# Performance work log

Hardware: AMD Instinct MI355X
Metric: run time of the kernel (lower is better)

Reference implementation:

```python
import jax, jax.numpy as jnp
import numpy as np

EMBED_DIM = 768
NUM_HEADS = 12
HEAD_DIM = EMBED_DIM // NUM_HEADS
SCALING = HEAD_DIM ** -0.5
B, N = 4, 2048


def setup_inputs() -> dict:
    key = jax.random.key(0)
    k_x, k_wqkv, k_bqkv, k_wo, k_bo = jax.random.split(key, 5)
    s = EMBED_DIM ** -0.5
    return {
        "x_q": jax.random.normal(k_x, (B, N, EMBED_DIM), dtype=jnp.float32),
        # torch Linear weight layout: (out_features, in_features)
        "w_qkv": jax.random.normal(k_wqkv, (3 * EMBED_DIM, EMBED_DIM), dtype=jnp.float32) * s,
        "b_qkv": jax.random.normal(k_bqkv, (3 * EMBED_DIM,), dtype=jnp.float32) * s,
        "w_out": jax.random.normal(k_wo, (EMBED_DIM, EMBED_DIM), dtype=jnp.float32) * s,
        "b_out": jax.random.normal(k_bo, (EMBED_DIM,), dtype=jnp.float32) * s,
    }


def reference(x_q, w_qkv, b_qkv, w_out, b_out):
    b_sz, n, _ = x_q.shape
    # qkv projection: x @ W^T + b -> (B, N, 3E)
    qkv = jnp.einsum("bne,fe->bnf", x_q, w_qkv) + b_qkv
    # reshape to (B, N, 3, H, D) then move heads: (B, H, 3, N, D)
    qkv = qkv.reshape(b_sz, n, 3, NUM_HEADS, HEAD_DIM).transpose(0, 3, 2, 1, 4)
    q, k, v = qkv[:, :, 0], qkv[:, :, 1], qkv[:, :, 2]
    q = q * SCALING
    # scores (B, H, N, N); att_m == 'Aug' adds constant +1 bias
    attn = jnp.einsum("bhqd,bhkd->bhqk", q, k) + 1.0
    attn = jax.nn.softmax(attn, axis=-1)
    # attn_dropout p=0.0 -> identity
    out = jnp.einsum("bhqk,bhkd->bhqd", attn, v)
    out = out.transpose(0, 2, 1, 3).reshape(b_sz, n, EMBED_DIM)
    return jnp.einsum("bne,fe->bnf", out, w_out) + b_out
```

## Files before the change

kernel.cpp:

```cpp
#include <hip/hip_runtime.h>

typedef unsigned short u16;
typedef unsigned int   u32;
typedef __bf16 bf16x4 __attribute__((ext_vector_type(4)));
typedef __bf16 bf16x8 __attribute__((ext_vector_type(8)));
typedef float  f32x4  __attribute__((ext_vector_type(4)));

__device__ __forceinline__ u16 f2bf(float f) {
  u32 u = __float_as_uint(f);
  u32 r = (u + 0x7fffu + ((u >> 16) & 1u)) >> 16;
  return (u16)r;
}

__device__ __forceinline__ float fexp2(float x) {
  return __builtin_amdgcn_exp2f(x);
}

typedef const __attribute__((address_space(1))) u32* gp1;
typedef __attribute__((address_space(3))) u32* lp3;
__device__ __forceinline__ void gload16(const void* g, void* l) {
  __builtin_amdgcn_global_load_lds((gp1)g, (lp3)l, 16, 0, 0);
}

__device__ __forceinline__ f32x4 mfma16(bf16x8 a, bf16x8 b, f32x4 c) {
  return __builtin_amdgcn_mfma_f32_16x16x32_bf16(a, b, c, 0, 0, 0);
}

__device__ __forceinline__ int swz8(int r) { return (r ^ (r >> 3)) & 7; }

__global__ __launch_bounds__(256) void cast_all(const float* __restrict__ x,
                                                const float* __restrict__ wqkv,
                                                const float* __restrict__ wo,
                                                uint4* __restrict__ dst) {
  int i = blockIdx.x * 256 + threadIdx.x;
  if (i >= 1081344) return;
  const float* s;
  int j;
  if (i < 786432)       { s = x;    j = i; }
  else if (i < 1007616) { s = wqkv; j = i - 786432; }
  else                  { s = wo;   j = i - 1007616; }
  const float4* s4 = (const float4*)s;
  float4 a = s4[2 * j], b = s4[2 * j + 1];
  uint4 o;
  o.x = (u32)f2bf(a.x) | ((u32)f2bf(a.y) << 16);
  o.y = (u32)f2bf(a.z) | ((u32)f2bf(a.w) << 16);
  o.z = (u32)f2bf(b.x) | ((u32)f2bf(b.y) << 16);
  o.w = (u32)f2bf(b.z) | ((u32)f2bf(b.w) << 16);
  dst[i] = o;
}

__global__ __launch_bounds__(256) void gemm_qkv(
    const u16* __restrict__ A, const u16* __restrict__ Bm,
    const float* __restrict__ bias,
    u16* __restrict__ Q, u16* __restrict__ K, u16* __restrict__ V) {
  __shared__ u16 As[2][128 * 64];
  __shared__ u16 Bs[2][128 * 64];
  const int tid = threadIdx.x, w = tid >> 6, l = tid & 63;
  const int lr = l & 15, lg = l >> 4;
  int id = blockIdx.x;
  int bi = (id & 7) * 144 + (id >> 3);
  const int m0 = (bi / 18) * 128, n0 = (bi % 18) * 128;
  const int wr = (w >> 1) * 64, wc = (w & 1) * 64;
  f32x4 acc[4][4] = {};

#define GSTAGE(buf, kt)                                                        \
  do {                                                                         \
    const u16* Ab = A + m0 * 768 + (kt);                                       \
    const u16* Bb = Bm + n0 * 768 + (kt);                                      \
    _Pragma("unroll") for (int i = 0; i < 4; ++i) {                            \
      int c = i * 256 + tid;                                                   \
      int r = c >> 3, q = c & 7;                                               \
      int qs = (q ^ swz8(r)) << 3;                                             \
      gload16(Ab + r * 768 + qs, (char*)As[buf] + c * 16);                     \
      gload16(Bb + r * 768 + qs, (char*)Bs[buf] + c * 16);                     \
    }                                                                          \
  } while (0)

  GSTAGE(0, 0);
  __syncthreads();

  for (int t = 0; t < 12; ++t) {
    const int buf = t & 1;
    if (t < 11) GSTAGE(buf ^ 1, (t + 1) * 64);
    bf16x8 af[4][2], bfr[4][2];
#pragma unroll
    for (int m = 0; m < 4; ++m) {
      int row = wr + m * 16 + lr;
      int sw = swz8(row);
#pragma unroll
      for (int ks = 0; ks < 2; ++ks)
        af[m][ks] = *(const bf16x8*)((char*)As[buf] + row * 128 +
                                     (((ks * 4 + lg) ^ sw) << 4));
    }
#pragma unroll
    for (int n = 0; n < 4; ++n) {
      int row = wc + n * 16 + lr;
      int sw = swz8(row);
#pragma unroll
      for (int ks = 0; ks < 2; ++ks)
        bfr[n][ks] = *(const bf16x8*)((char*)Bs[buf] + row * 128 +
                                      (((ks * 4 + lg) ^ sw) << 4));
    }
    __builtin_amdgcn_s_setprio(1);
#pragma unroll
    for (int ks = 0; ks < 2; ++ks)
#pragma unroll
      for (int m = 0; m < 4; ++m)
#pragma unroll
        for (int n = 0; n < 4; ++n)
          acc[m][n] = mfma16(af[m][ks], bfr[n][ks], acc[m][n]);
    __builtin_amdgcn_s_setprio(0);
    __syncthreads();
  }

#pragma unroll
  for (int n = 0; n < 4; ++n) {
    int f = n0 + wc + n * 16 + lr;
    float bv = bias[f];
    int three = f / 768;
    int hd = f - three * 768;
    int h = hd >> 6, dd = hd & 63;
    if (three == 2) {
#pragma unroll
      for (int m = 0; m < 4; ++m) {
        int row0 = m0 + wr + m * 16 + lg * 4;
        int b2 = row0 >> 11, ns = row0 & 2047;
        ushort4 pk;
        pk.x = f2bf(acc[m][n][0] + bv);
        pk.y = f2bf(acc[m][n][1] + bv);
        pk.z = f2bf(acc[m][n][2] + bv);
        pk.w = f2bf(acc[m][n][3] + bv);
        *(ushort4*)&V[((size_t)(b2 * 12 + h) * 64 + dd) * 2048 + ns] = pk;
      }
    } else {
      u16* dst = (three == 0) ? Q : K;
      float sc = (three == 0) ? 0.125f * 1.44269504f : 1.0f;
#pragma unroll
      for (int m = 0; m < 4; ++m) {
        int row0 = m0 + wr + m * 16 + lg * 4;
#pragma unroll
        for (int j = 0; j < 4; ++j) {
          int row = row0 + j;
          int b2 = row >> 11, ns = row & 2047;
          float val = (acc[m][n][j] + bv) * sc;
          dst[(((b2 * 12 + h) * 2048 + ns) << 6) + dd] = f2bf(val);
        }
      }
    }
  }
}

__global__ __launch_bounds__(256, 3) void attn_kernel(
    const u16* __restrict__ Q, const u16* __restrict__ K,
    const u16* __restrict__ Vt, u16* __restrict__ O) {
  __shared__ u16 Ks[3][64 * 64];
  __shared__ u16 Vs[3][64 * 64];
  const int tid = threadIdx.x, w = tid >> 6, l = tid & 63;
  const int lr = l & 15, lg = l >> 4;
  int d0i = blockIdx.x;
  int bi = (d0i & 7) * 96 + (d0i >> 3);
  int qt = bi & 15, h = (bi >> 4) % 12, b = bi / 192;
  const u16* Qp = Q + ((size_t)(b * 12 + h) * 2048 + qt * 128) * 64;
  const u16* Kp = K + (size_t)(b * 12 + h) * 2048 * 64;
  const u16* Vp = Vt + (size_t)(b * 12 + h) * 64 * 2048;
  u16* Op = O + (size_t)(b * 2048 + qt * 128) * 768 + h * 64;

  bf16x8 aq[2][2];
#pragma unroll
  for (int mt = 0; mt < 2; ++mt)
#pragma unroll
    for (int ks = 0; ks < 2; ++ks)
      aq[mt][ks] = *(const bf16x8*)&Qp[(w * 32 + mt * 16 + lr) * 64 + ks * 32 + lg * 8];

  bf16x8 vone;
#pragma unroll
  for (int i = 0; i < 8; ++i) vone[i] = (__bf16)1.0f;

  f32x4 aO[2][4] = {};
  f32x4 sacc[2] = {};

#define STAGEP(kb, vb, kt)                                                     \
  do {                                                                         \
    const u16* Kt = Kp + (kt) * 4096;                                          \
    const u16* Vg = Vp + (kt) * 64;                                            \
    _Pragma("unroll") for (int i = 0; i < 2; ++i) {                            \
      int c = i * 256 + tid;                                                   \
      int r = c >> 3, q = c & 7;                                               \
      int qs = (q ^ swz8(r)) << 3;                                             \
      gload16(Kt + r * 64 + qs, (char*)(kb) + c * 16);                         \
      gload16(Vg + r * 2048 + qs, (char*)(vb) + c * 16);                       \
    }                                                                          \
  } while (0)

  u16 *kc = Ks[0], *kn = Ks[1], *kf = Ks[2];
  u16 *vc = Vs[0], *vn = Vs[1], *vf = Vs[2];

  STAGEP(kc, vc, 0);
  STAGEP(kn, vn, 1);

  for (int kt = 0; kt < 32; ++kt) {
    if (kt == 31) asm volatile("s_waitcnt vmcnt(0)" ::: "memory");
    else          asm volatile("s_waitcnt vmcnt(4)" ::: "memory");
    __builtin_amdgcn_s_barrier();
    __builtin_amdgcn_sched_barrier(0);
    if (kt < 30) STAGEP(kf, vf, kt + 2);

    f32x4 S[2][4] = {};
    __builtin_amdgcn_s_setprio(1);
#pragma unroll
    for (int nt = 0; nt < 4; ++nt) {
      int row = nt * 16 + lr;
      int sw = swz8(row);
#pragma unroll
      for (int ks = 0; ks < 2; ++ks) {
        bf16x8 a = *(const bf16x8*)((char*)kc + row * 128 +
                                    (((ks * 4 + lg) ^ sw) << 4));
        S[0][nt] = mfma16(a, aq[0][ks], S[0][nt]);
        S[1][nt] = mfma16(a, aq[1][ks], S[1][nt]);
      }
    }
    __builtin_amdgcn_s_setprio(0);

    bf16x8 ap[2][2];
#pragma unroll
    for (int mt = 0; mt < 2; ++mt) {
      f32x4 pe[4];
#pragma unroll
      for (int nt = 0; nt < 4; ++nt)
#pragma unroll
        for (int j = 0; j < 4; ++j) pe[nt][j] = fexp2(S[mt][nt][j]);
#pragma unroll
      for (int ks = 0; ks < 2; ++ks) {
        bf16x8 f;
#pragma unroll
        for (int j = 0; j < 4; ++j) {
          f[j]     = (__bf16)pe[2 * ks][j];
          f[4 + j] = (__bf16)pe[2 * ks + 1][j];
        }
        ap[mt][ks] = f;
      }
    }

    __builtin_amdgcn_s_setprio(1);
#pragma unroll
    for (int ks = 0; ks < 2; ++ks) {
      sacc[0] = mfma16(ap[0][ks], vone, sacc[0]);
      sacc[1] = mfma16(ap[1][ks], vone, sacc[1]);
#pragma unroll
      for (int dt = 0; dt < 4; ++dt) {
        int row = dt * 16 + lr;
        int sw = swz8(row);
        char* vrow = (char*)vc + row * 128 + (lg & 1) * 8;
        bf16x4 lo = *(const bf16x4*)(vrow + (((ks * 4 + (lg >> 1)) ^ sw) << 4));
        bf16x4 hi = *(const bf16x4*)(vrow + (((ks * 4 + 2 + (lg >> 1)) ^ sw) << 4));
        bf16x8 bv = __builtin_shufflevector(lo, hi, 0, 1, 2, 3, 4, 5, 6, 7);
        aO[0][dt] = mfma16(ap[0][ks], bv, aO[0][dt]);
        aO[1][dt] = mfma16(ap[1][ks], bv, aO[1][dt]);
      }
    }
    __builtin_amdgcn_s_setprio(0);

    u16* tk = kc; kc = kn; kn = kf; kf = tk;
    u16* tv = vc; vc = vn; vn = vf; vf = tv;
  }

#pragma unroll
  for (int mt = 0; mt < 2; ++mt) {
    f32x4 rinv;
#pragma unroll
    for (int j = 0; j < 4; ++j) rinv[j] = 1.0f / sacc[mt][j];
#pragma unroll
    for (int dt = 0; dt < 4; ++dt)
#pragma unroll
      for (int j = 0; j < 4; ++j) {
        int row = w * 32 + mt * 16 + lg * 4 + j;
        Op[(size_t)row * 768 + dt * 16 + lr] = f2bf(aO[mt][dt][j] * rinv[j]);
      }
  }
}

__global__ __launch_bounds__(256) void gemm_out(
    const u16* __restrict__ A, const u16* __restrict__ Bm,
    const float* __restrict__ bias, float* __restrict__ C) {
  __shared__ u16 As[2][128 * 64];
  __shared__ u16 Bs[2][128 * 64];
  const int tid = threadIdx.x, w = tid >> 6, l = tid & 63;
  const int lr = l & 15, lg = l >> 4;
  int id = blockIdx.x;
  int bi = (id & 7) * 48 + (id >> 3);
  const int m0 = (bi / 6) * 128, n0 = (bi % 6) * 128;
  const int wr = (w >> 1) * 64, wc = (w & 1) * 64;
  f32x4 acc[4][4] = {};

  GSTAGE(0, 0);
  __syncthreads();

  for (int t = 0; t < 12; ++t) {
    const int buf = t & 1;
    if (t < 11) GSTAGE(buf ^ 1, (t + 1) * 64);
    bf16x8 af[4][2], bfr[4][2];
#pragma unroll
    for (int m = 0; m < 4; ++m) {
      int row = wr + m * 16 + lr;
      int sw = swz8(row);
#pragma unroll
      for (int ks = 0; ks < 2; ++ks)
        af[m][ks] = *(const bf16x8*)((char*)As[buf] + row * 128 +
                                     (((ks * 4 + lg) ^ sw) << 4));
    }
#pragma unroll
    for (int n = 0; n < 4; ++n) {
      int row = wc + n * 16 + lr;
      int sw = swz8(row);
#pragma unroll
      for (int ks = 0; ks < 2; ++ks)
        bfr[n][ks] = *(const bf16x8*)((char*)Bs[buf] + row * 128 +
                                      (((ks * 4 + lg) ^ sw) << 4));
    }
    __builtin_amdgcn_s_setprio(1);
#pragma unroll
    for (int ks = 0; ks < 2; ++ks)
#pragma unroll
      for (int m = 0; m < 4; ++m)
#pragma unroll
        for (int n = 0; n < 4; ++n)
          acc[m][n] = mfma16(af[m][ks], bfr[n][ks], acc[m][n]);
    __builtin_amdgcn_s_setprio(0);
    __syncthreads();
  }

#pragma unroll
  for (int n = 0; n < 4; ++n) {
    int f = n0 + wc + n * 16 + lr;
    float bv = bias[f];
#pragma unroll
    for (int m = 0; m < 4; ++m) {
      int row0 = m0 + wr + m * 16 + lg * 4;
#pragma unroll
      for (int j = 0; j < 4; ++j) {
        int row = row0 + j;
        C[(size_t)row * 768 + f] = acc[m][n][j] + bv;
      }
    }
  }
}

extern "C" void kernel_launch(void* const* d_in, const int* in_sizes, int n_in,
                              void* d_out, int out_size, void* d_ws, size_t ws_size,
                              hipStream_t stream) {
  const float* x     = (const float*)d_in[0];
  const float* w_qkv = (const float*)d_in[1];
  const float* b_qkv = (const float*)d_in[2];
  const float* w_out = (const float*)d_in[3];
  const float* b_out = (const float*)d_in[4];

  char* ws = (char*)d_ws;
  u16* xb    = (u16*)(ws + 0);
  u16* wqkvb = (u16*)(ws + 12582912);
  u16* wob   = (u16*)(ws + 16121856);
  u16* qb    = (u16*)(ws + 17301504);
  u16* kb    = (u16*)(ws + 29884416);
  u16* vb    = (u16*)(ws + 42467328);
  u16* ob    = (u16*)(ws + 55050240);

  cast_all<<<4224, 256, 0, stream>>>(x, w_qkv, w_out, (uint4*)ws);

  gemm_qkv<<<1152, 256, 0, stream>>>(xb, wqkvb, b_qkv, qb, kb, vb);
  attn_kernel<<<768, 256, 0, stream>>>(qb, kb, vb, ob);
  gemm_out<<<384, 256, 0, stream>>>(ob, wob, b_out, (float*)d_out);
}
```

Measured before the change: 132.2 us.

## Triple-buffer GEMM K-loops with BK=32 and halve gemm_out N tile

Both projection GEMMs move from a double-buffered BK=64 loop with __syncthreads to a three-stage ring of BK=32 tiles. Each iteration waits with an explicit vmcnt and a single barrier, then prefetches two stages ahead, so global loads overlap more MFMA work and LDS per block shrinks, letting three blocks fit per CU. gemm_out also changes from 128x128 to 128x64 output tiles and launches 768 blocks, improving CU fill for the small output GEMM. The cost is twice as many barriers per K, a new row-pair swizzled LDS layout that must be conflict-free, and hand-tuned vmcnt counts that must match the number of outstanding loads.

New measurement: 138.7 us. 4.9% more time.

```diff
diff --git a/kernel.cpp b/kernel.cpp
--- a/kernel.cpp
+++ b/kernel.cpp
@@ -49,12 +49,13 @@
   dst[i] = o;
 }
 
-__global__ __launch_bounds__(256) void gemm_qkv(
+
+__global__ __launch_bounds__(256, 3) void gemm_qkv(
     const u16* __restrict__ A, const u16* __restrict__ Bm,
     const float* __restrict__ bias,
     u16* __restrict__ Q, u16* __restrict__ K, u16* __restrict__ V) {
-  __shared__ u16 As[2][128 * 64];
-  __shared__ u16 Bs[2][128 * 64];
+  __shared__ u16 As[3][64 * 64];
+  __shared__ u16 Bs[3][64 * 64];
   const int tid = threadIdx.x, w = tid >> 6, l = tid & 63;
   const int lr = l & 15, lg = l >> 4;
   int id = blockIdx.x;
@@ -63,54 +64,56 @@
   const int wr = (w >> 1) * 64, wc = (w & 1) * 64;
   f32x4 acc[4][4] = {};
 
-#define GSTAGE(buf, kt)                                                        \
+#define QSTAGE(ab, bb, kt)                                                     \
   do {                                                                         \
     const u16* Ab = A + m0 * 768 + (kt);                                       \
     const u16* Bb = Bm + n0 * 768 + (kt);                                      \
-    _Pragma("unroll") for (int i = 0; i < 4; ++i) {                            \
+    _Pragma("unroll") for (int i = 0; i < 2; ++i) {                            \
       int c = i * 256 + tid;                                                   \
-      int r = c >> 3, q = c & 7;                                               \
-      int qs = (q ^ swz8(r)) << 3;                                             \
-      gload16(Ab + r * 768 + qs, (char*)As[buf] + c * 16);                     \
-      gload16(Bb + r * 768 + qs, (char*)Bs[buf] + c * 16);                     \
+      int vr = c >> 3;                                                         \
+      int chl = (c & 7) ^ swz8(vr);                                            \
+      int r = vr * 2 + (chl >> 2), col = (chl & 3) * 8;                        \
+      gload16(Ab + r * 768 + col, (char*)(ab) + c * 16);                       \
+      gload16(Bb + r * 768 + col, (char*)(bb) + c * 16);                       \
     }                                                                          \
   } while (0)
 
-  GSTAGE(0, 0);
-  __syncthreads();
-
-  for (int t = 0; t < 12; ++t) {
-    const int buf = t & 1;
-    if (t < 11) GSTAGE(buf ^ 1, (t + 1) * 64);
-    bf16x8 af[4][2], bfr[4][2];
+  u16 *aC = As[0], *aN = As[1], *aF = As[2];
+  u16 *bC = Bs[0], *bN = Bs[1], *bF = Bs[2];
+  QSTAGE(aC, bC, 0);
+  QSTAGE(aN, bN, 32);
+
+  for (int t = 0; t < 24; ++t) {
+    if (t == 23) asm volatile("s_waitcnt vmcnt(0)" ::: "memory");
+    else         asm volatile("s_waitcnt vmcnt(4)" ::: "memory");
+    __builtin_amdgcn_s_barrier();
+    __builtin_amdgcn_sched_barrier(0);
+    if (t < 22) QSTAGE(aF, bF, (t + 2) * 32);
+
+    bf16x8 fa[4], fb[4];
 #pragma unroll
     for (int m = 0; m < 4; ++m) {
       int row = wr + m * 16 + lr;
-      int sw = swz8(row);
-#pragma unroll
-      for (int ks = 0; ks < 2; ++ks)
-        af[m][ks] = *(const bf16x8*)((char*)As[buf] + row * 128 +
-                                     (((ks * 4 + lg) ^ sw) << 4));
+      int vr = row >> 1;
+      int chs = (((row & 1) << 2) | lg) ^ swz8(vr);
+      fa[m] = *(const bf16x8*)((char*)aC + vr * 128 + (chs << 4));
     }
 #pragma unroll
     for (int n = 0; n < 4; ++n) {
       int row = wc + n * 16 + lr;
-      int sw = swz8(row);
-#pragma unroll
-      for (int ks = 0; ks < 2; ++ks)
-        bfr[n][ks] = *(const bf16x8*)((char*)Bs[buf] + row * 128 +
-                                      (((ks * 4 + lg) ^ sw) << 4));
+      int vr = row >> 1;
+      int chs = (((row & 1) << 2) | lg) ^ swz8(vr);
+      fb[n] = *(const bf16x8*)((char*)bC + vr * 128 + (chs << 4));
     }
     __builtin_amdgcn_s_setprio(1);
 #pragma unroll
-    for (int ks = 0; ks < 2; ++ks)
-#pragma unroll
-      for (int m = 0; m < 4; ++m)
-#pragma unroll
-        for (int n = 0; n < 4; ++n)
-          acc[m][n] = mfma16(af[m][ks], bfr[n][ks], acc[m][n]);
+    for (int m = 0; m < 4; ++m)
+#pragma unroll
+      for (int n = 0; n < 4; ++n) acc[m][n] = mfma16(fa[m], fb[n], acc[m][n]);
     __builtin_amdgcn_s_setprio(0);
-    __syncthreads();
+
+    u16* ta = aC; aC = aN; aN = aF; aF = ta;
+    u16* tb = bC; bC = bN; bN = bF; bF = tb;
   }
 
 #pragma unroll
@@ -279,58 +282,79 @@
   }
 }
 
-__global__ __launch_bounds__(256) void gemm_out(
+__global__ __launch_bounds__(256, 3) void gemm_out(
     const u16* __restrict__ A, const u16* __restrict__ Bm,
     const float* __restrict__ bias, float* __restrict__ C) {
-  __shared__ u16 As[2][128 * 64];
-  __shared__ u16 Bs[2][128 * 64];
+  __shared__ u16 As[3][64 * 64];
+  __shared__ u16 Bs[3][32 * 64];
   const int tid = threadIdx.x, w = tid >> 6, l = tid & 63;
   const int lr = l & 15, lg = l >> 4;
   int id = blockIdx.x;
-  int bi = (id & 7) * 48 + (id >> 3);
-  const int m0 = (bi / 6) * 128, n0 = (bi % 6) * 128;
-  const int wr = (w >> 1) * 64, wc = (w & 1) * 64;
-  f32x4 acc[4][4] = {};
-
-  GSTAGE(0, 0);
-  __syncthreads();
-
-  for (int t = 0; t < 12; ++t) {
-    const int buf = t & 1;
-    if (t < 11) GSTAGE(buf ^ 1, (t + 1) * 64);
-    bf16x8 af[4][2], bfr[4][2];
+  int bi = (id & 7) * 96 + (id >> 3);
+  const int m0 = (bi / 12) * 128, n0 = (bi % 12) * 64;
+  const int wr = (w >> 1) * 64, wc = (w & 1) * 32;
+  f32x4 acc[4][2] = {};
+
+#define OSTAGE(ab, bb, kt)                                                     \
+  do {                                                                         \
+    const u16* Ab = A + m0 * 768 + (kt);                                       \
+    const u16* Bb = Bm + n0 * 768 + (kt);                                      \
+    _Pragma("unroll") for (int i = 0; i < 2; ++i) {                            \
+      int c = i * 256 + tid;                                                   \
+      int vr = c >> 3;                                                         \
+      int chl = (c & 7) ^ swz8(vr);                                            \
+      int r = vr * 2 + (chl >> 2), col = (chl & 3) * 8;                        \
+      gload16(Ab + r * 768 + col, (char*)(ab) + c * 16);                       \
+    }                                                                          \
+    {                                                                          \
+      int c = tid;                                                             \
+      int vr = c >> 3;                                                         \
+      int chl = (c & 7) ^ swz8(vr);                                            \
+      int r = vr * 2 + (chl >> 2), col = (chl & 3) * 8;                        \
+      gload16(Bb + r * 768 + col, (char*)(bb) + c * 16);                       \
+    }                                                                          \
+  } while (0)
+
+  u16 *aC = As[0], *aN = As[1], *aF = As[2];
+  u16 *bC = Bs[0], *bN = Bs[1], *bF = Bs[2];
+  OSTAGE(aC, bC, 0);
+  OSTAGE(aN, bN, 32);
+
+  for (int t = 0; t < 24; ++t) {
+    if (t == 23) asm volatile("s_waitcnt vmcnt(0)" ::: "memory");
+    else         asm volatile("s_waitcnt vmcnt(3)" ::: "memory");
+    __builtin_amdgcn_s_barrier();
+    __builtin_amdgcn_sched_barrier(0);
+    if (t < 22) OSTAGE(aF, bF, (t + 2) * 32);
+
+    bf16x8 fa[4], fb[2];
 #pragma unroll
     for (int m = 0; m < 4; ++m) {
       int row = wr + m * 16 + lr;
-      int sw = swz8(row);
-#pragma unroll
-      for (int ks = 0; ks < 2; ++ks)
-        af[m][ks] = *(const bf16x8*)((char*)As[buf] + row * 128 +
-                                     (((ks * 4 + lg) ^ sw) << 4));
-    }
-#pragma unroll
-    for (int n = 0; n < 4; ++n) {
+      int vr = row >> 1;
+      int chs = (((row & 1) << 2) | lg) ^ swz8(vr);
+      fa[m] = *(const bf16x8*)((char*)aC + vr * 128 + (chs << 4));
+    }
+#pragma unroll
+    for (int n = 0; n < 2; ++n) {
       int row = wc + n * 16 + lr;
-      int sw = swz8(row);
-#pragma unroll
-      for (int ks = 0; ks < 2; ++ks)
-        bfr[n][ks] = *(const bf16x8*)((char*)Bs[buf] + row * 128 +
-                                      (((ks * 4 + lg) ^ sw) << 4));
+      int vr = row >> 1;
+      int chs = (((row & 1) << 2) | lg) ^ swz8(vr);
+      fb[n] = *(const bf16x8*)((char*)bC + vr * 128 + (chs << 4));
     }
     __builtin_amdgcn_s_setprio(1);
 #pragma unroll
-    for (int ks = 0; ks < 2; ++ks)
-#pragma unroll
-      for (int m = 0; m < 4; ++m)
-#pragma unroll
-        for (int n = 0; n < 4; ++n)
-          acc[m][n] = mfma16(af[m][ks], bfr[n][ks], acc[m][n]);
+    for (int m = 0; m < 4; ++m)
+#pragma unroll
+      for (int n = 0; n < 2; ++n) acc[m][n] = mfma16(fa[m], fb[n], acc[m][n]);
     __builtin_amdgcn_s_setprio(0);
-    __syncthreads();
-  }
-
-#pragma unroll
-  for (int n = 0; n < 4; ++n) {
+
+    u16* ta = aC; aC = aN; aN = aF; aF = ta;
+    u16* tb = bC; bC = bN; bN = bF; bF = tb;
+  }
+
+#pragma unroll
+  for (int n = 0; n < 2; ++n) {
     int f = n0 + wc + n * 16 + lr;
     float bv = bias[f];
 #pragma unroll
@@ -367,5 +391,5 @@
 
   gemm_qkv<<<1152, 256, 0, stream>>>(xb, wqkvb, b_qkv, qb, kb, vb);
   attn_kernel<<<768, 256, 0, stream>>>(qb, kb, vb, ob);
-  gemm_out<<<384, 256, 0, stream>>>(ob, wob, b_out, (float*)d_out);
-}
+  gemm_out<<<768, 256, 0, stream>>>(ob, wob, b_out, (float*)d_out);
+}
```
